# Optimization experiments

Measured on AMD Instinct MI355X. Metric: run time of the kernel, lower is better.

## Reference

```python
import jax, jax.numpy as jnp
import numpy as np

B, C, IC, H, W = 4, 256, 128, 64, 64
EPS = 1e-5  # BatchNorm eps (eval mode, running stats)


def conv_bn(x, w, b, gamma, beta, mean, var, relu):
    # 1x1 conv == channel contraction; BN in eval mode (affine w/ running stats)
    y = jnp.einsum('oc,bchw->bohw', w, x) + b[None, :, None, None]
    scale = gamma * jax.lax.rsqrt(var + EPS)
    shift = beta - mean * scale
    y = y * scale[None, :, None, None] + shift[None, :, None, None]
    return jax.nn.relu(y) if relu else y


def setup_inputs() -> dict:
    key = jax.random.key(0)
    ks = jax.random.split(key, 32)

    def branch(i, co, ci):
        return dict(
            w=jax.random.normal(ks[i], (co, ci), jnp.float32) * 0.05,
            b=jax.random.normal(ks[i + 1], (co,), jnp.float32) * 0.05,
            gamma=jax.random.uniform(ks[i + 2], (co,), jnp.float32, 0.5, 1.5),
            beta=jax.random.normal(ks[i + 3], (co,), jnp.float32) * 0.05,
            mean=jax.random.normal(ks[i + 4], (co,), jnp.float32) * 0.05,
            var=jax.random.uniform(ks[i + 5], (co,), jnp.float32, 0.5, 1.5),
        )

    g = branch(0, IC, C)
    th = branch(6, IC, C)
    ph = branch(12, IC, C)
    wo = branch(18, C, IC)
    inp = {'x': jax.random.normal(ks[24], (B, C, H, W), jnp.float32)}
    for pre, p in (('g', g), ('th', th), ('ph', ph), ('w', wo)):
        for k, v in p.items():
            inp[f'{pre}_{k}'] = v
    return inp


def reference(x, g_w, g_b, g_gamma, g_beta, g_mean, g_var,
              th_w, th_b, th_gamma, th_beta, th_mean, th_var,
              ph_w, ph_b, ph_gamma, ph_beta, ph_mean, ph_var,
              w_w, w_b, w_gamma, w_beta, w_mean, w_var):
    b, c, h, w = x.shape
    ic = g_w.shape[0]
    g_x = conv_bn(x, g_w, g_b, g_gamma, g_beta, g_mean, g_var, True).reshape(b, ic, h * w)     # [b,ic,n]
    theta = conv_bn(x, th_w, th_b, th_gamma, th_beta, th_mean, th_var, True).reshape(b, ic, h * w)
    phi = conv_bn(x, ph_w, ph_b, ph_gamma, ph_beta, ph_mean, ph_var, True).reshape(b, ic, h * w)
    # unscaled attention over flattened spatial positions
    f = jnp.einsum('bcn,bcm->bnm', theta, phi)     # [b,n,n]
    a = jax.nn.softmax(f, axis=2)
    y = jnp.einsum('bnm,bcm->bcn', a, g_x)         # [b,ic,n]
    y = y.reshape(b, ic, h, w)
    y = conv_bn(y, w_w, w_b, w_gamma, w_beta, w_mean, w_var, False)
    return y + x
```

## Files before the change

kernel.cpp:

```cpp
#include <hip/hip_runtime.h>
#include <math.h>

typedef __attribute__((ext_vector_type(8))) short short8;
typedef __attribute__((ext_vector_type(8))) _Float16 half8;
typedef __attribute__((ext_vector_type(4))) float f32x4;
typedef __attribute__((ext_vector_type(16))) float f32x16;

#define NSP 4096
#define CIN 256
#define ICH 128
#define SPLITS 4
#define TILES_PER_SPLIT 16
#define LOG2E 1.44269504088896f

__device__ __forceinline__ unsigned short f2h(float x){
  union { _Float16 h; unsigned short u; } v; v.h = (_Float16)x; return v.u;
}
__device__ __forceinline__ float h2f(unsigned short u){
  union { _Float16 h; unsigned short u; } v; v.u = u; return (float)v.h;
}
__device__ __forceinline__ unsigned pk2h(float a, float b){
  union { __fp16 __attribute__((ext_vector_type(2))) v; unsigned u; } r;
  r.v = __builtin_amdgcn_cvt_pkrtz(a, b);
  return r.u;
}
__device__ __forceinline__ float fexp2(float x){
  float r;
  asm("v_exp_f32 %0, %1" : "=v"(r) : "v"(x));
  return r;
}
__device__ __forceinline__ int swz(int row, int e){ return e ^ ((row & 7) << 3); }
__device__ __forceinline__ int swzK(int row, int e){ return e ^ ((row & 15) << 3); }

__device__ __forceinline__ f32x4 mfmah(short8 a, short8 b, f32x4 c){
  union { short8 s; half8 h; } ua, ub; ua.s = a; ub.s = b;
  return __builtin_amdgcn_mfma_f32_16x16x32_f16(ua.h, ub.h, c, 0, 0, 0);
}
__device__ __forceinline__ f32x16 mfma32(short8 a, short8 b, f32x16 c){
  union { short8 s; half8 h; } ua, ub; ua.s = a; ub.s = b;
  return __builtin_amdgcn_mfma_f32_32x32x16_f16(ua.h, ub.h, c, 0, 0, 0);
}

__device__ __forceinline__ void gload_lds16(const unsigned short* g, unsigned short* l){
  __builtin_amdgcn_global_load_lds(
      (const __attribute__((address_space(1))) unsigned int*)g,
      (__attribute__((address_space(3))) unsigned int*)l, 16, 0, 0);
}

__device__ __forceinline__ void stage_nc(const unsigned short* gbase, unsigned short* lds,
                                         int w, int l){
  #pragma unroll
  for (int i=0;i<4;++i){
    int rl = 16*w + 4*i + (l>>4);
    int eg = ((l&15)*8) ^ ((rl&15)<<3);
    gload_lds16(gbase + (size_t)rl*128 + eg, lds + w*2048 + i*512);
  }
}

__device__ __forceinline__ int kperm(int q){
  int m = q & 15;
  return (q & 16) | (((m>>2)&1)<<3) | (m&3) | (((m>>3)&1)<<2);
}

__global__ __launch_bounds__(256) void conv_fused_k(
    const float* __restrict__ x,
    const float* __restrict__ w0, const float* __restrict__ b0,
    const float* __restrict__ ga0, const float* __restrict__ be0,
    const float* __restrict__ me0, const float* __restrict__ va0,
    const float* __restrict__ w1, const float* __restrict__ b1,
    const float* __restrict__ ga1, const float* __restrict__ be1,
    const float* __restrict__ me1, const float* __restrict__ va1,
    const float* __restrict__ w2, const float* __restrict__ b2,
    const float* __restrict__ ga2, const float* __restrict__ be2,
    const float* __restrict__ me2, const float* __restrict__ va2,
    unsigned short* __restrict__ outg, unsigned short* __restrict__ outt,
    unsigned short* __restrict__ outp)
{
  const int b = blockIdx.z, nt = blockIdx.x, ot = blockIdx.y;
  const int n0 = nt*64, o0 = ot*64;
  const int t = threadIdx.x, w = t>>6, l = t&63;
  __shared__ unsigned short xs[64][64];
  __shared__ unsigned short ws[3][64][64];
  __shared__ float sc_s[3][64], sh_s[3][64];
  if (t < 64){
    int o = o0 + t;
    float s0 = ga0[o]*rsqrtf(va0[o]+1e-5f);
    sc_s[0][t]=s0; sh_s[0][t]=be0[o]-me0[o]*s0+b0[o]*s0;
    float s1 = ga1[o]*rsqrtf(va1[o]+1e-5f);
    sc_s[1][t]=s1*LOG2E; sh_s[1][t]=(be1[o]-me1[o]*s1+b1[o]*s1)*LOG2E;
    float s2 = ga2[o]*rsqrtf(va2[o]+1e-5f);
    sc_s[2][t]=s2; sh_s[2][t]=be2[o]-me2[o]*s2+b2[o]*s2;
  }
  const f32x4 Z = {0.f,0.f,0.f,0.f};
  f32x4 acc[3][4];
  #pragma unroll
  for (int br=0;br<3;++br) for (int i=0;i<4;++i) acc[br][i] = Z;
  const float* Wt[3] = {w0, w1, w2};

  for (int kc = 0; kc < CIN; kc += 64){
    __syncthreads();
    #pragma unroll
    for (int p2 = 0; p2 < 2; ++p2){
      int cpr = p2*32 + 2*(t>>4);
      int nb = (t&15)*4;
      const float* xr0 = x + ((size_t)b*CIN + kc + cpr)*NSP + n0 + nb;
      float4 xa = *(const float4*)xr0;
      float4 xb = *(const float4*)(xr0 + NSP);
      float aa[4] = {xa.x, xa.y, xa.z, xa.w};
      float bb[4] = {xb.x, xb.y, xb.z, xb.w};
      #pragma unroll
      for (int i=0;i<4;++i){
        int r = nb + i;
        *(unsigned*)&xs[r][swz(r, cpr)] = pk2h(aa[i], bb[i]);
      }
    }
    #pragma unroll
    for (int p = 0; p < 4; ++p){
      int cw = p*16 + (t>>4);
      int q4 = (t&15)*4;
      #pragma unroll
      for (int br=0;br<3;++br){
        float4 wv = *(const float4*)(Wt[br] + (size_t)(o0 + cw)*CIN + kc + q4);
        uint2 u; u.x = pk2h(wv.x, wv.y); u.y = pk2h(wv.z, wv.w);
        *(uint2*)&ws[br][cw][swz(cw, q4)] = u;
      }
    }
    __syncthreads();
    #pragma unroll
    for (int kf = 0; kf < 2; ++kf){
      int ko = kf*32 + (l>>4)*8;
      int wr = 16*w + (l&15);
      short8 wf0 = *(const short8*)&ws[0][wr][swz(wr, ko)];
      short8 wf1 = *(const short8*)&ws[1][wr][swz(wr, ko)];
      short8 wf2 = *(const short8*)&ws[2][wr][swz(wr, ko)];
      #pragma unroll
      for (int nf = 0; nf < 4; ++nf){
        int xr = 16*nf + (l&15);
        short8 xf = *(const short8*)&xs[xr][swz(xr, ko)];
        acc[0][nf] = mfmah(wf0, xf, acc[0][nf]);
        acc[1][nf] = mfmah(xf, wf1, acc[1][nf]);
        acc[2][nf] = mfmah(xf, wf2, acc[2][nf]);
      }
    }
  }
  #pragma unroll
  for (int j=0;j<4;++j){
    int ol = 16*w + (l>>4)*4 + j;
    float s = sc_s[0][ol], sh = sh_s[0][ol];
    #pragma unroll
    for (int nf=0;nf<4;++nf){
      int n = n0 + 16*nf + (l&15);
      int nst = (n & ~31) | kperm(n & 31);
      float v = fmaxf(acc[0][nf][j]*s + sh, 0.f);
      outg[((size_t)b*ICH + o0 + ol)*NSP + nst] = f2h(v);
    }
  }
  {
    int ol = 16*w + (l&15);
    float s1 = sc_s[1][ol], sh1 = sh_s[1][ol];
    float s2 = sc_s[2][ol], sh2 = sh_s[2][ol];
    #pragma unroll
    for (int nf=0; nf<4; ++nf)
      #pragma unroll
      for (int j=0;j<4;++j){
        int n = n0 + 16*nf + (l>>4)*4 + j;
        float v1 = fmaxf(acc[1][nf][j]*s1 + sh1, 0.f);
        float v2 = fmaxf(acc[2][nf][j]*s2 + sh2, 0.f);
        outt[((size_t)b*NSP + n)*ICH + o0 + ol] = f2h(v1);
        outp[((size_t)b*NSP + n)*ICH + o0 + ol] = f2h(v2);
      }
  }
}

__global__ __launch_bounds__(256, 2) void attn_k(
  const unsigned short* __restrict__ thp, const unsigned short* __restrict__ php,
  const unsigned short* __restrict__ gb, unsigned short* __restrict__ ypart,
  float* __restrict__ ml)
{
  const int bx = blockIdx.x;
  const int xcd = bx & 7, jj = bx >> 3;
  const int combo = xcd*2 + (jj>>5);
  const int qt = jj & 31;
  const int b = combo & 3, s = combo >> 2;
  const int n0 = qt*128;
  const int t = threadIdx.x, w = t>>6, l = t&63;
  const int hi = l>>5, ln = l&31;

  __shared__ unsigned short kb[2][8192];
  __shared__ unsigned short vb[2][8192];

  stage_nc(thp + ((size_t)b*NSP + n0      )*ICH, &kb[0][0], w, l);
  stage_nc(thp + ((size_t)b*NSP + n0 + 64 )*ICH, &kb[1][0], w, l);
  __syncthreads();
  short8 qf[8];
  {
    const unsigned short* qsrc = (w >> 1) ? &kb[1][0] : &kb[0][0];
    int r = 32*(w & 1) + ln;
    #pragma unroll
    for (int kc=0;kc<8;++kc)
      qf[kc] = *(const short8*)&qsrc[r*128 + swzK(r, kc*16 + 8*hi)];
  }
  __syncthreads();

  f32x16 oa[4];
  #pragma unroll
  for (int i=0;i<4;++i)
    #pragma unroll
    for (int j=0;j<16;++j) oa[i][j] = 0.f;
  float mr = -1e30f, lr = 0.f;
  unsigned pk[16];

  const int tile0 = s*TILES_PER_SPLIT;

  const unsigned short* kp[4];
  const unsigned short* vp[4];
  {
    const unsigned short* kbase = php + ((size_t)b*NSP + tile0*64)*ICH;
    const unsigned short* vbase = gb + (size_t)b*ICH*NSP + tile0*64;
    #pragma unroll
    for (int i=0;i<4;++i){
      int rl = 16*w + 4*i + (l>>4);
      int eg = ((l&15)*8) ^ ((rl&15)<<3);
      kp[i] = kbase + (size_t)rl*128 + eg;
      int cl = 32*w + 8*i + (l>>3);
      int me = ((l&7)*8) ^ ((cl&7)<<3);
      vp[i] = vbase + (size_t)cl*NSP + me;
    }
  }
  {
    unsigned short* kd = &kb[0][0] + w*2048;
    unsigned short* vd = &vb[0][0] + w*2048;
    #pragma unroll
    for (int i=0;i<4;++i){
      gload_lds16(kp[i], kd + i*512); kp[i] += 64*ICH;
      gload_lds16(vp[i], vd + i*512); vp[i] += 64;
    }
  }
  __syncthreads();
  int cur = 0;

  for (int it = 0; it < TILES_PER_SPLIT; ++it){
    if (it < TILES_PER_SPLIT-1){
      unsigned short* kd = &kb[cur^1][0] + w*2048;
      unsigned short* vd = &vb[cur^1][0] + w*2048;
      #pragma unroll
      for (int i=0;i<4;++i){
        gload_lds16(kp[i], kd + i*512); kp[i] += 64*ICH;
        gload_lds16(vp[i], vd + i*512); vp[i] += 64;
      }
    }

    f32x16 sc0, sc1;
    #pragma unroll
    for (int j=0;j<16;++j){ sc0[j]=0.f; sc1[j]=0.f; }
    __builtin_amdgcn_s_setprio(1);
    #pragma unroll
    for (int kc=0;kc<8;++kc){
      int eo = kc*16 + 8*hi;
      short8 a0 = *(const short8*)&kb[cur][(ln     )*128 + swzK(ln,      eo)];
      short8 a1 = *(const short8*)&kb[cur][(32 + ln)*128 + swzK(32 + ln, eo)];
      sc0 = mfma32(a0, qf[kc], sc0);
      sc1 = mfma32(a1, qf[kc], sc1);
    }
    __builtin_amdgcn_s_setprio(0);

    {
      float t0 = fmaxf(fmaxf(sc0[0],sc0[1]),  fmaxf(sc0[2],sc0[3]));
      float t1 = fmaxf(fmaxf(sc0[4],sc0[5]),  fmaxf(sc0[6],sc0[7]));
      float t2 = fmaxf(fmaxf(sc0[8],sc0[9]),  fmaxf(sc0[10],sc0[11]));
      float t3 = fmaxf(fmaxf(sc0[12],sc0[13]),fmaxf(sc0[14],sc0[15]));
      float t4 = fmaxf(fmaxf(sc1[0],sc1[1]),  fmaxf(sc1[2],sc1[3]));
      float t5 = fmaxf(fmaxf(sc1[4],sc1[5]),  fmaxf(sc1[6],sc1[7]));
      float t6 = fmaxf(fmaxf(sc1[8],sc1[9]),  fmaxf(sc1[10],sc1[11]));
      float t7 = fmaxf(fmaxf(sc1[12],sc1[13]),fmaxf(sc1[14],sc1[15]));
      float mx = fmaxf(fmaxf(fmaxf(t0,t1),fmaxf(t2,t3)),
                       fmaxf(fmaxf(t4,t5),fmaxf(t6,t7)));
      mx = fmaxf(mx, __shfl_xor(mx, 32));
      if (__any(mx - mr > 11.5f)){
        float mn = fmaxf(mr, mx);
        float al = fexp2(mr - mn);
        mr = mn; lr *= al;
        #pragma unroll
        for (int j=0;j<16;++j){
          int rowj = (j&3) + 8*(j>>2) + 4*hi;
          float alj = __shfl(al, rowj);
          #pragma unroll
          for (int ct=0;ct<4;++ct) oa[ct][j] *= alj;
        }
      }
    }

    float sA=0.f, sB=0.f, sC=0.f, sD=0.f;
    #pragma unroll
    for (int r=0;r<16;r+=4){
      sc0[r]   = fexp2(sc0[r]  -mr); sA += sc0[r];
      sc0[r+1] = fexp2(sc0[r+1]-mr); sB += sc0[r+1];
      sc0[r+2] = fexp2(sc0[r+2]-mr); sC += sc0[r+2];
      sc0[r+3] = fexp2(sc0[r+3]-mr); sD += sc0[r+3];
    }
    #pragma unroll
    for (int s2=0;s2<2;++s2)
      #pragma unroll
      for (int q=0;q<4;++q)
        pk[s2*4+q] = pk2h(sc0[8*s2+2*q], sc0[8*s2+2*q+1]);
    __builtin_amdgcn_s_setprio(1);
    #pragma unroll
    for (int s2=0;s2<2;++s2){
      union { unsigned u[4]; short8 s8; } au;
      #pragma unroll
      for (int q=0;q<4;++q) au.u[q] = pk[4*s2+q];
      int eo = 16*s2 + 8*hi;
      #pragma unroll
      for (int ct=0;ct<4;++ct){
        int cr = 32*ct + ln;
        short8 bv = *(const short8*)&vb[cur][cr*64 + swz(cr, eo)];
        oa[ct] = mfma32(au.s8, bv, oa[ct]);
      }
    }
    __builtin_amdgcn_s_setprio(0);
    #pragma unroll
    for (int r=0;r<16;r+=4){
      sc1[r]   = fexp2(sc1[r]  -mr); sA += sc1[r];
      sc1[r+1] = fexp2(sc1[r+1]-mr); sB += sc1[r+1];
      sc1[r+2] = fexp2(sc1[r+2]-mr); sC += sc1[r+2];
      sc1[r+3] = fexp2(sc1[r+3]-mr); sD += sc1[r+3];
    }
    #pragma unroll
    for (int s2=0;s2<2;++s2)
      #pragma unroll
      for (int q=0;q<4;++q)
        pk[8+s2*4+q] = pk2h(sc1[8*s2+2*q], sc1[8*s2+2*q+1]);
    lr += (sA + sB) + (sC + sD);
    __builtin_amdgcn_s_setprio(1);
    #pragma unroll
    for (int s2=0;s2<2;++s2){
      union { unsigned u[4]; short8 s8; } au;
      #pragma unroll
      for (int q=0;q<4;++q) au.u[q] = pk[8+4*s2+q];
      int eo = 32 + 16*s2 + 8*hi;
      #pragma unroll
      for (int ct=0;ct<4;++ct){
        int cr = 32*ct + ln;
        short8 bv = *(const short8*)&vb[cur][cr*64 + swz(cr, eo)];
        oa[ct] = mfma32(au.s8, bv, oa[ct]);
      }
    }
    __builtin_amdgcn_s_setprio(0);

    __syncthreads();
    cur ^= 1;
  }

  lr += __shfl_xor(lr, 32);
  float invl = 1.f / lr;
  #pragma unroll
  for (int j=0;j<16;++j){
    int rowj = (j&3) + 8*(j>>2) + 4*hi;
    float invj = __shfl(invl, rowj);
    int n = n0 + 32*w + rowj;
    #pragma unroll
    for (int ct=0;ct<4;++ct){
      int c = 32*ct + ln;
      ypart[(((size_t)s*4 + b)*NSP + n)*ICH + c] = f2h(oa[ct][j]*invj);
    }
  }
  if (l < 32){
    int n = n0 + 32*w + l;
    ml[(((size_t)s*4 + b)*NSP + n)*2 + 0] = mr;
    ml[(((size_t)s*4 + b)*NSP + n)*2 + 1] = lr;
  }
}

__global__ __launch_bounds__(256) void final_k2(
  const unsigned short* __restrict__ ypart, const float* __restrict__ ml,
  const float* __restrict__ x, const float* __restrict__ Wm,
  const float* __restrict__ bias, const float* __restrict__ gamma,
  const float* __restrict__ beta, const float* __restrict__ mean,
  const float* __restrict__ var, float* __restrict__ out)
{
  const int b = blockIdx.z, oth = blockIdx.y, nt = blockIdx.x;
  const int n0 = nt*64, obase = oth*128;
  const int t = threadIdx.x, w = t>>6, l = t&63;
  __shared__ unsigned short ys[64][128];
  __shared__ unsigned short w2s[64][128];
  __shared__ float wc[SPLITS][64];
  __shared__ float sc_s[128], sh_s[128];
  if (t < 128){
    int o = obase + t;
    float s = gamma[o]*rsqrtf(var[o]+1e-5f);
    sc_s[t]=s; sh_s[t]=beta[o]-mean[o]*s+bias[o]*s;
  } else if (t < 192){
    int r = t - 128, n = n0 + r;
    float mv[SPLITS], lv[SPLITS];
    #pragma unroll
    for (int s=0;s<SPLITS;++s){
      mv[s] = ml[(((size_t)s*4 + b)*NSP + n)*2 + 0];
      lv[s] = ml[(((size_t)s*4 + b)*NSP + n)*2 + 1];
    }
    float M = fmaxf(fmaxf(mv[0],mv[1]), fmaxf(mv[2],mv[3]));
    float wsum = 0.f, wv[SPLITS];
    #pragma unroll
    for (int s=0;s<SPLITS;++s){ wv[s] = lv[s]*exp2f(mv[s]-M); wsum += wv[s]; }
    float inv = 1.f/wsum;
    #pragma unroll
    for (int s=0;s<SPLITS;++s) wc[s][r] = wv[s]*inv;
  }
  __syncthreads();
  #pragma unroll
  for (int p=0;p<4;++p){
    int id = p*256 + t, r = id>>4, c8 = (id&15)*8;
    float accv[8] = {0,0,0,0,0,0,0,0};
    #pragma unroll
    for (int s=0;s<SPLITS;++s){
      short8 v = *(const short8*)(ypart + (((size_t)s*4 + b)*NSP + n0 + r)*ICH + c8);
      float wgt = wc[s][r];
      #pragma unroll
      for (int i=0;i<8;++i) accv[i] += wgt * h2f(((unsigned short*)&v)[i]);
    }
    unsigned short hv[8];
    #pragma unroll
    for (int i=0;i<8;++i) hv[i] = f2h(accv[i]);
    *(short8*)&ys[r][swz(r,c8)] = *(short8*)hv;
  }

  const f32x4 Z = {0.f,0.f,0.f,0.f};
  #pragma unroll
  for (int ot2 = 0; ot2 < 2; ++ot2){
    const int o0 = obase + ot2*64;
    #pragma unroll
    for (int p=0;p<4;++p){
      int id = p*256 + t, r = id>>4, c8 = (id&15)*8;
      float4 u0 = *(const float4*)(Wm + (size_t)(o0 + r)*ICH + c8);
      float4 u1 = *(const float4*)(Wm + (size_t)(o0 + r)*ICH + c8 + 4);
      unsigned short wh[8] = {f2h(u0.x),f2h(u0.y),f2h(u0.z),f2h(u0.w),
                              f2h(u1.x),f2h(u1.y),f2h(u1.z),f2h(u1.w)};
      *(short8*)&w2s[r][swz(r,c8)] = *(short8*)wh;
    }
    __syncthreads();
    f32x4 acc[4];
    #pragma unroll
    for (int i=0;i<4;++i) acc[i]=Z;
    #pragma unroll
    for (int kf=0;kf<4;++kf){
      int ko = kf*32 + (l>>4)*8;
      int wr = 16*w + (l&15);
      short8 a = *(const short8*)&w2s[wr][swz(wr,ko)];
      #pragma unroll
      for (int nf=0;nf<4;++nf){
        int yr = 16*nf + (l&15);
        short8 bb = *(const short8*)&ys[yr][swz(yr,ko)];
        acc[nf] = mfmah(a, bb, acc[nf]);
      }
    }
    #pragma unroll
    for (int j=0;j<4;++j){
      int ol = 16*w + (l>>4)*4 + j;
      float s = sc_s[ot2*64 + ol], sh = sh_s[ot2*64 + ol];
      #pragma unroll
      for (int nf=0;nf<4;++nf){
        int n = n0 + 16*nf + (l&15);
        size_t idx = ((size_t)b*CIN + o0 + ol)*NSP + n;
        out[idx] = acc[nf][j]*s + sh + x[idx];
      }
    }
    __syncthreads();
  }
}

extern "C" void kernel_launch(void* const* d_in, const int* in_sizes, int n_in,
                              void* d_out, int out_size, void* d_ws, size_t ws_size,
                              hipStream_t stream){
  const float* x    = (const float*)d_in[0];
  const float* g_w  = (const float*)d_in[1];
  const float* g_b  = (const float*)d_in[2];
  const float* g_ga = (const float*)d_in[3];
  const float* g_be = (const float*)d_in[4];
  const float* g_me = (const float*)d_in[5];
  const float* g_va = (const float*)d_in[6];
  const float* t_w  = (const float*)d_in[7];
  const float* t_b  = (const float*)d_in[8];
  const float* t_ga = (const float*)d_in[9];
  const float* t_be = (const float*)d_in[10];
  const float* t_me = (const float*)d_in[11];
  const float* t_va = (const float*)d_in[12];
  const float* p_w  = (const float*)d_in[13];
  const float* p_b  = (const float*)d_in[14];
  const float* p_ga = (const float*)d_in[15];
  const float* p_be = (const float*)d_in[16];
  const float* p_me = (const float*)d_in[17];
  const float* p_va = (const float*)d_in[18];
  const float* w_w  = (const float*)d_in[19];
  const float* w_b  = (const float*)d_in[20];
  const float* w_ga = (const float*)d_in[21];
  const float* w_be = (const float*)d_in[22];
  const float* w_me = (const float*)d_in[23];
  const float* w_va = (const float*)d_in[24];

  char* ws = (char*)d_ws;
  const size_t SEG = (size_t)4*NSP*ICH*sizeof(unsigned short);
  unsigned short* th_t  = (unsigned short*)(ws);
  unsigned short* ph_t  = (unsigned short*)(ws + SEG);
  unsigned short* g_cn  = (unsigned short*)(ws + 2*SEG);
  unsigned short* ypart = (unsigned short*)(ws + 3*SEG);
  float*          mlb   = (float*)(ws + 3*SEG + SPLITS*SEG);

  dim3 blk(256,1,1);
  conv_fused_k<<<dim3(64,2,4), blk, 0, stream>>>(
      x,
      g_w, g_b, g_ga, g_be, g_me, g_va,
      t_w, t_b, t_ga, t_be, t_me, t_va,
      p_w, p_b, p_ga, p_be, p_me, p_va,
      g_cn, th_t, ph_t);
  attn_k<<<dim3(512,1,1), blk, 0, stream>>>(th_t, ph_t, g_cn, ypart, mlb);
  final_k2<<<dim3(64,2,4), blk, 0, stream>>>(ypart, mlb, x, w_w, w_b, w_ga, w_be, w_me, w_va, (float*)d_out);
}
```

Before: 69.10 us.

## Double attention splits and widen attention blocks to 512 threads with 256 queries

Raises the key-split count from 4 to 8 and halves the tiles per split. Each attention block now has 8 waves covering 256 query rows, with the K/V staging loops rebalanced across the extra waves. The Q staging reuses all four LDS buffers. The merge kernel generalizes its max reduction to the new split count, and the weight conversion in the final kernel uses packed half conversion. More splits means more partial outputs to write and merge, and the larger blocks raise register and occupancy pressure.

Result: slower. 119.9 us (+73.5%).

```diff
diff --git a/kernel.cpp b/kernel.cpp
--- a/kernel.cpp
+++ b/kernel.cpp
@@ -9,8 +9,8 @@
 #define NSP 4096
 #define CIN 256
 #define ICH 128
-#define SPLITS 4
-#define TILES_PER_SPLIT 16
+#define SPLITS 8
+#define TPS 8
 #define LOG2E 1.44269504088896f
 
 __device__ __forceinline__ unsigned short f2h(float x){
@@ -45,16 +45,6 @@
   __builtin_amdgcn_global_load_lds(
       (const __attribute__((address_space(1))) unsigned int*)g,
       (__attribute__((address_space(3))) unsigned int*)l, 16, 0, 0);
-}
-
-__device__ __forceinline__ void stage_nc(const unsigned short* gbase, unsigned short* lds,
-                                         int w, int l){
-  #pragma unroll
-  for (int i=0;i<4;++i){
-    int rl = 16*w + 4*i + (l>>4);
-    int eg = ((l&15)*8) ^ ((rl&15)<<3);
-    gload_lds16(gbase + (size_t)rl*128 + eg, lds + w*2048 + i*512);
-  }
 }
 
 __device__ __forceinline__ int kperm(int q){
@@ -172,30 +162,48 @@
   }
 }
 
-__global__ __launch_bounds__(256, 2) void attn_k(
+__global__ __launch_bounds__(512, 4) void attn_k(
   const unsigned short* __restrict__ thp, const unsigned short* __restrict__ php,
   const unsigned short* __restrict__ gb, unsigned short* __restrict__ ypart,
   float* __restrict__ ml)
 {
   const int bx = blockIdx.x;
   const int xcd = bx & 7, jj = bx >> 3;
-  const int combo = xcd*2 + (jj>>5);
-  const int qt = jj & 31;
+  const int combo = xcd*4 + (jj>>4);
+  const int qt = jj & 15;
   const int b = combo & 3, s = combo >> 2;
-  const int n0 = qt*128;
+  const int n0 = qt*256;
   const int t = threadIdx.x, w = t>>6, l = t&63;
   const int hi = l>>5, ln = l&31;
 
-  __shared__ unsigned short kb[2][8192];
-  __shared__ unsigned short vb[2][8192];
-
-  stage_nc(thp + ((size_t)b*NSP + n0      )*ICH, &kb[0][0], w, l);
-  stage_nc(thp + ((size_t)b*NSP + n0 + 64 )*ICH, &kb[1][0], w, l);
+  __shared__ unsigned short kb0a[8192];
+  __shared__ unsigned short kb1a[8192];
+  __shared__ unsigned short vb0a[8192];
+  __shared__ unsigned short vb1a[8192];
+  unsigned short* kb0 = kb0a;
+  unsigned short* kb1 = kb1a;
+  unsigned short* vb0 = vb0a;
+  unsigned short* vb1 = vb1a;
+  auto qsel = [&](int c) -> unsigned short* {
+    return c==0 ? kb0 : (c==1 ? kb1 : (c==2 ? vb0 : vb1));
+  };
+
+  #pragma unroll
+  for (int c=0;c<4;++c){
+    const unsigned short* src = thp + ((size_t)b*NSP + n0 + c*64)*ICH;
+    unsigned short* dst = qsel(c) + w*1024;
+    #pragma unroll
+    for (int i=0;i<2;++i){
+      int rl = 8*w + 4*i + (l>>4);
+      int eg = ((l&15)*8) ^ ((rl&15)<<3);
+      gload_lds16(src + (size_t)rl*128 + eg, dst + i*512);
+    }
+  }
   __syncthreads();
   short8 qf[8];
   {
-    const unsigned short* qsrc = (w >> 1) ? &kb[1][0] : &kb[0][0];
-    int r = 32*(w & 1) + ln;
+    const unsigned short* qsrc = qsel(w>>1);
+    int r = 32*(w&1) + ln;
     #pragma unroll
     for (int kc=0;kc<8;++kc)
       qf[kc] = *(const short8*)&qsrc[r*128 + swzK(r, kc*16 + 8*hi)];
@@ -210,28 +218,28 @@
   float mr = -1e30f, lr = 0.f;
   unsigned pk[16];
 
-  const int tile0 = s*TILES_PER_SPLIT;
-
-  const unsigned short* kp[4];
-  const unsigned short* vp[4];
+  const int tile0 = s*TPS;
+
+  const unsigned short* kp[2];
+  const unsigned short* vp[2];
   {
     const unsigned short* kbase = php + ((size_t)b*NSP + tile0*64)*ICH;
     const unsigned short* vbase = gb + (size_t)b*ICH*NSP + tile0*64;
     #pragma unroll
-    for (int i=0;i<4;++i){
-      int rl = 16*w + 4*i + (l>>4);
+    for (int i=0;i<2;++i){
+      int rl = 8*w + 4*i + (l>>4);
       int eg = ((l&15)*8) ^ ((rl&15)<<3);
       kp[i] = kbase + (size_t)rl*128 + eg;
-      int cl = 32*w + 8*i + (l>>3);
+      int cl = 16*w + 8*i + (l>>3);
       int me = ((l&7)*8) ^ ((cl&7)<<3);
       vp[i] = vbase + (size_t)cl*NSP + me;
     }
   }
   {
-    unsigned short* kd = &kb[0][0] + w*2048;
-    unsigned short* vd = &vb[0][0] + w*2048;
-    #pragma unroll
-    for (int i=0;i<4;++i){
+    unsigned short* kd = kb0 + w*1024;
+    unsigned short* vd = vb0 + w*1024;
+    #pragma unroll
+    for (int i=0;i<2;++i){
       gload_lds16(kp[i], kd + i*512); kp[i] += 64*ICH;
       gload_lds16(vp[i], vd + i*512); vp[i] += 64;
     }
@@ -239,12 +247,14 @@
   __syncthreads();
   int cur = 0;
 
-  for (int it = 0; it < TILES_PER_SPLIT; ++it){
-    if (it < TILES_PER_SPLIT-1){
-      unsigned short* kd = &kb[cur^1][0] + w*2048;
-      unsigned short* vd = &vb[cur^1][0] + w*2048;
-      #pragma unroll
-      for (int i=0;i<4;++i){
+  for (int it = 0; it < TPS; ++it){
+    unsigned short* kcur = cur ? kb1 : kb0;
+    unsigned short* vcur = cur ? vb1 : vb0;
+    if (it < TPS-1){
+      unsigned short* kd = (cur ? kb0 : kb1) + w*1024;
+      unsigned short* vd = (cur ? vb0 : vb1) + w*1024;
+      #pragma unroll
+      for (int i=0;i<2;++i){
         gload_lds16(kp[i], kd + i*512); kp[i] += 64*ICH;
         gload_lds16(vp[i], vd + i*512); vp[i] += 64;
       }
@@ -257,8 +267,8 @@
     #pragma unroll
     for (int kc=0;kc<8;++kc){
       int eo = kc*16 + 8*hi;
-      short8 a0 = *(const short8*)&kb[cur][(ln     )*128 + swzK(ln,      eo)];
-      short8 a1 = *(const short8*)&kb[cur][(32 + ln)*128 + swzK(32 + ln, eo)];
+      short8 a0 = *(const short8*)&kcur[(ln     )*128 + swzK(ln,      eo)];
+      short8 a1 = *(const short8*)&kcur[(32 + ln)*128 + swzK(32 + ln, eo)];
       sc0 = mfma32(a0, qf[kc], sc0);
       sc1 = mfma32(a1, qf[kc], sc1);
     }
@@ -313,7 +323,7 @@
       #pragma unroll
       for (int ct=0;ct<4;++ct){
         int cr = 32*ct + ln;
-        short8 bv = *(const short8*)&vb[cur][cr*64 + swz(cr, eo)];
+        short8 bv = *(const short8*)&vcur[cr*64 + swz(cr, eo)];
         oa[ct] = mfma32(au.s8, bv, oa[ct]);
       }
     }
@@ -341,7 +351,7 @@
       #pragma unroll
       for (int ct=0;ct<4;++ct){
         int cr = 32*ct + ln;
-        short8 bv = *(const short8*)&vb[cur][cr*64 + swz(cr, eo)];
+        short8 bv = *(const short8*)&vcur[cr*64 + swz(cr, eo)];
         oa[ct] = mfma32(au.s8, bv, oa[ct]);
       }
     }
@@ -397,7 +407,9 @@
       mv[s] = ml[(((size_t)s*4 + b)*NSP + n)*2 + 0];
       lv[s] = ml[(((size_t)s*4 + b)*NSP + n)*2 + 1];
     }
-    float M = fmaxf(fmaxf(mv[0],mv[1]), fmaxf(mv[2],mv[3]));
+    float M = mv[0];
+    #pragma unroll
+    for (int s=1;s<SPLITS;++s) M = fmaxf(M, mv[s]);
     float wsum = 0.f, wv[SPLITS];
     #pragma unroll
     for (int s=0;s<SPLITS;++s){ wv[s] = lv[s]*exp2f(mv[s]-M); wsum += wv[s]; }
@@ -432,9 +444,10 @@
       int id = p*256 + t, r = id>>4, c8 = (id&15)*8;
       float4 u0 = *(const float4*)(Wm + (size_t)(o0 + r)*ICH + c8);
       float4 u1 = *(const float4*)(Wm + (size_t)(o0 + r)*ICH + c8 + 4);
-      unsigned short wh[8] = {f2h(u0.x),f2h(u0.y),f2h(u0.z),f2h(u0.w),
-                              f2h(u1.x),f2h(u1.y),f2h(u1.z),f2h(u1.w)};
-      *(short8*)&w2s[r][swz(r,c8)] = *(short8*)wh;
+      uint2 u; u.x = pk2h(u0.x, u0.y); u.y = pk2h(u0.z, u0.w);
+      uint2 v2; v2.x = pk2h(u1.x, u1.y); v2.y = pk2h(u1.z, u1.w);
+      *(uint2*)&w2s[r][swz(r,c8)] = u;
+      *(uint2*)&w2s[r][swz(r,c8)+4] = v2;
     }
     __syncthreads();
     f32x4 acc[4];
@@ -511,6 +524,6 @@
       t_w, t_b, t_ga, t_be, t_me, t_va,
       p_w, p_b, p_ga, p_be, p_me, p_va,
       g_cn, th_t, ph_t);
-  attn_k<<<dim3(512,1,1), blk, 0, stream>>>(th_t, ph_t, g_cn, ypart, mlb);
+  attn_k<<<dim3(512,1,1), dim3(512,1,1), 0, stream>>>(th_t, ph_t, g_cn, ypart, mlb);
   final_k2<<<dim3(64,2,4), blk, 0, stream>>>(ypart, mlb, x, w_w, w_b, w_ga, w_be, w_me, w_va, (float*)d_out);
 }
```
